# Optimization experiments

Measured on AMD Instinct MI355X. Metric: run time of the kernel, lower is better.

Reference implementation:

```python
import jax, jax.numpy as jnp
import numpy as np
from jax import lax

# MuSc core (post-ViT): multiscale avg-pooled patch features -> mutual pairwise
# distance scoring (leave-one-out over batch) -> top-min-k mean -> pixel map.
L_LAYERS = 4      # len(feature_layers)
B = 8             # batch (mutual-scoring reference pool)
PH = PW = 24      # 336 / patch 14
P = PH * PW       # 576 patches
D = 1024          # ViT-L embed dim
H = W = 336       # input image size
R_LIST = (1, 3, 5)
TOPMIN_MIN = 0.0
TOPMIN_MAX = 0.3


def setup_inputs() -> dict:
    key = jax.random.key(0)
    features = jax.random.normal(key, (L_LAYERS, B, P, D), dtype=jnp.float32)
    return {"features": features}


def _avg_pool_r(x, r):
    # x: [L, B, P, D]; AvgPool2d(r, stride=1, pad=r//2, count_include_pad=True)
    if r == 1:
        return x
    Ln, Bn, Pn, Dn = x.shape
    g = x.reshape(Ln, Bn, PH, PW, Dn)
    pad = r // 2
    s = lax.reduce_window(g, 0.0, lax.add,
                          (1, 1, r, r, 1), (1, 1, 1, 1, 1),
                          ((0, 0), (0, 0), (pad, pad), (pad, pad), (0, 0)))
    return (s / (r * r)).reshape(Ln, Bn, Pn, Dn)


def _msm_scores(feat):
    # feat: [L, B, P, D] L2-normalized. Mutual scoring (leave-one-out over B).
    sq = jnp.sum(feat * feat, axis=-1)                       # [L,B,P]
    dots = jnp.einsum('lbpd,lcqd->lbpcq', feat, feat)        # [L,B,P,B,P]
    d2 = sq[:, :, :, None, None] + sq[:, None, None, :, :] - 2.0 * dots
    d = jnp.sqrt(jnp.maximum(d2, 0.0))
    dmin = jnp.min(d, axis=-1)                               # [L,B,P,C] min over ref patches
    self_mask = jnp.eye(B, dtype=bool)[:, None, :]           # [B,1,C] exclude self image
    dmin = jnp.where(self_mask[None], jnp.inf, dmin)
    ds = jnp.sort(dmin, axis=-1)                             # ascending; self (inf) last
    ref = B - 1
    k_min = int(TOPMIN_MIN * ref)
    k_max = max(int(TOPMIN_MAX * ref), k_min + 1)
    return jnp.mean(ds[..., k_min:k_max], axis=-1)           # [L,B,P]


def _bilinear_ac(x, out_h, out_w):
    # align_corners=True bilinear upsample, x: [B, ph, pw]
    Bn, ph, pw = x.shape
    ys = jnp.arange(out_h, dtype=jnp.float32) * ((ph - 1) / (out_h - 1))
    xs = jnp.arange(out_w, dtype=jnp.float32) * ((pw - 1) / (out_w - 1))
    y0 = jnp.floor(ys).astype(jnp.int32); y1 = jnp.minimum(y0 + 1, ph - 1)
    x0 = jnp.floor(xs).astype(jnp.int32); x1 = jnp.minimum(x0 + 1, pw - 1)
    wy = (ys - y0)[None, :, None]
    wx = (xs - x0)[None, None, :]
    f00 = x[:, y0[:, None], x0[None, :]]
    f01 = x[:, y0[:, None], x1[None, :]]
    f10 = x[:, y1[:, None], x0[None, :]]
    f11 = x[:, y1[:, None], x1[None, :]]
    return (f00 * (1 - wy) * (1 - wx) + f01 * (1 - wy) * wx
            + f10 * wy * (1 - wx) + f11 * wy * wx)


def _forward(features):
    scores_r = []
    for r in R_LIST:  # small fixed multiscale loop
        f = _avg_pool_r(features, r)
        f = f / jnp.linalg.norm(f, axis=-1, keepdims=True)
        s = _msm_scores(f)                    # [L,B,P]
        scores_r.append(jnp.mean(s, axis=0))  # [B,P] mean over layers
    scores = jnp.mean(jnp.stack(scores_r, 0), axis=0)  # [B,P] mean over r
    scores_image = jnp.max(scores, axis=1)              # [B]
    scores_pixel = _bilinear_ac(scores.reshape(-1, PH, PW), H, W)  # [B,H,W]
    return scores_image, scores_pixel


def reference(features):
    return _forward(features)
```

## Files before the change

kernel.cpp:

```cpp
#include <hip/hip_runtime.h>
#include <stdint.h>

#define L_LAYERS 4
#define BATCH 8
#define PHH 24
#define PWW 24
#define PP (PHH*PWW)
#define DD 1024
#define ROWS (BATCH*PP)
#define OH 336
#define OW 336
#define NTILES 72
#define TT 36
#define NPAIRS (TT*(TT+1)/2)
#define NCOMBO 12
#define TOTBLK (NPAIRS*NCOMBO)
#define PRESCALE 1024.0f
#define INV_PRESCALE2_X2 (1.f/524288.f)

typedef __attribute__((ext_vector_type(8))) int i32x8;
typedef __attribute__((ext_vector_type(4))) float f32x4;

__device__ __forceinline__ unsigned int f2bf(float f) {
  unsigned int u = __float_as_uint(f);
  return (u + 0x7FFFu + ((u >> 16) & 1u)) >> 16;
}

__device__ __forceinline__ void load4bf(float* d, const unsigned short* p) {
  const uint2 u = *(const uint2*)p;
  d[0] = __uint_as_float(u.x << 16);
  d[1] = __uint_as_float(u.x & 0xFFFF0000u);
  d[2] = __uint_as_float(u.y << 16);
  d[3] = __uint_as_float(u.y & 0xFFFF0000u);
}

__device__ __forceinline__ void async16(const void* g, void* l) {
  __builtin_amdgcn_global_load_lds(
      (const __attribute__((address_space(1))) void*)(size_t)(uintptr_t)g,
      (__attribute__((address_space(3))) void*)(uint32_t)(uintptr_t)l,
      16, 0, 0);
}

__global__ __launch_bounds__(256) void vpool_ring_kernel(
    const float* __restrict__ feat,
    unsigned short* __restrict__ c3,
    unsigned short* __restrict__ c5) {
  const int dch = blockIdx.x;
  const int b = blockIdx.y;
  const int l = blockIdx.z >> 1;
  const int half = blockIdx.z & 1;
  const int py0 = half * 12, py1 = py0 + 11;
  const int t = threadIdx.x;
  const int pxg = t >> 5;
  const int d2 = t & 31;

  __shared__ float ring[5][24 * 64];

  const float* fb = feat + ((size_t)l * BATCH + b) * PP * DD + dch * 64 + d2 * 2;

  for (int yy = py0 - 2; yy <= py0 + 1; ++yy) {
    if (yy < 0) continue;
    #pragma unroll
    for (int i = 0; i < 3; ++i) {
      int px = i * 8 + pxg;
      *(float2*)&ring[yy % 5][px * 64 + d2 * 2] =
          *(const float2*)(fb + (size_t)(yy * PWW + px) * DD);
    }
  }
  for (int py = py0; py <= py1; ++py) {
    const int yl = py + 2;
    if (yl < PHH) {
      __syncthreads();
      #pragma unroll
      for (int i = 0; i < 3; ++i) {
        int px = i * 8 + pxg;
        *(float2*)&ring[yl % 5][px * 64 + d2 * 2] =
            *(const float2*)(fb + (size_t)(yl * PWW + px) * DD);
      }
    }
    __syncthreads();
    #pragma unroll
    for (int i = 0; i < 3; ++i) {
      int px = i * 8 + pxg;
      float s3x = 0.f, s3y = 0.f, s5x = 0.f, s5y = 0.f;
      #pragma unroll
      for (int dy = -2; dy <= 2; ++dy) {
        int yy = py + dy;
        if (yy < 0 || yy >= PHH) continue;
        float2 v = *(const float2*)&ring[yy % 5][px * 64 + d2 * 2];
        s5x += v.x; s5y += v.y;
        if (dy >= -1 && dy <= 1) { s3x += v.x; s3y += v.y; }
      }
      const size_t idx =
          ((size_t)l * ROWS + b * PP + py * PWW + px) * DD + dch * 64 + d2 * 2;
      *(unsigned int*)&c3[idx] = f2bf(s3x) | (f2bf(s3y) << 16);
      *(unsigned int*)&c5[idx] = f2bf(s5x) | (f2bf(s5y) << 16);
    }
  }
}

__global__ __launch_bounds__(256) void hpool_slide_kernel(
    const float* __restrict__ feat,
    const unsigned short* __restrict__ c3,
    const unsigned short* __restrict__ c5,
    unsigned char* __restrict__ nf_all) {
  const int rb = blockIdx.x;
  const int l = blockIdx.y;
  const int b = rb / PHH, py = rb % PHH;
  const int t = threadIdx.x;
  const int lane = t & 63, w = t >> 6;
  const int d0 = t * 4;
  const size_t rowbase = (size_t)b * PP + (size_t)py * PWW;

  const float* fb = feat + ((size_t)l * BATCH * PP + rowbase) * DD + d0;
  const unsigned short* c3b = c3 + ((size_t)l * ROWS + rowbase) * DD + d0;
  const unsigned short* c5b = c5 + ((size_t)l * ROWS + rowbase) * DD + d0;
  unsigned char* nf1 = nf_all + (((size_t)(0*L_LAYERS + l) * ROWS + rowbase) * DD + d0);
  unsigned char* nf3 = nf_all + (((size_t)(1*L_LAYERS + l) * ROWS + rowbase) * DD + d0);
  unsigned char* nf5 = nf_all + (((size_t)(2*L_LAYERS + l) * ROWS + rowbase) * DD + d0);

  float w3[3][4] = {{0,0,0,0},{0,0,0,0},{0,0,0,0}};
  float w5[5][4] = {{0,0,0,0},{0,0,0,0},{0,0,0,0},{0,0,0,0},{0,0,0,0}};
  load4bf(w3[1], c3b);
  load4bf(w3[2], c3b + DD);
  load4bf(w5[2], c5b);
  load4bf(w5[3], c5b + DD);
  load4bf(w5[4], c5b + 2 * DD);

  __shared__ float red[4][3];

  for (int px = 0; px < PWW; ++px) {
    float s1[4], s3[4], s5[4];
    const float4 f = *(const float4*)(fb + (size_t)px * DD);
    s1[0] = f.x; s1[1] = f.y; s1[2] = f.z; s1[3] = f.w;
    #pragma unroll
    for (int j = 0; j < 4; ++j) {
      s3[j] = w3[0][j] + w3[1][j] + w3[2][j];
      s5[j] = w5[0][j] + w5[1][j] + w5[2][j] + w5[3][j] + w5[4][j];
    }
    float q1 = 0, q3 = 0, q5 = 0;
    #pragma unroll
    for (int j = 0; j < 4; ++j) {
      q1 += s1[j]*s1[j]; q3 += s3[j]*s3[j]; q5 += s5[j]*s5[j];
    }
    #pragma unroll
    for (int off = 32; off > 0; off >>= 1) {
      q1 += __shfl_down(q1, off);
      q3 += __shfl_down(q3, off);
      q5 += __shfl_down(q5, off);
    }
    __syncthreads();
    if (lane == 0) { red[w][0] = q1; red[w][1] = q3; red[w][2] = q5; }
    __syncthreads();
    const float rn1 = rsqrtf(red[0][0] + red[1][0] + red[2][0] + red[3][0]) * PRESCALE;
    const float rn3 = rsqrtf(red[0][1] + red[1][1] + red[2][1] + red[3][1]) * PRESCALE;
    const float rn5 = rsqrtf(red[0][2] + red[1][2] + red[2][2] + red[3][2]) * PRESCALE;

    const size_t po = (size_t)px * DD;
    unsigned int o;
    o = __builtin_amdgcn_cvt_pk_fp8_f32(s1[0]*rn1, s1[1]*rn1, 0, false);
    o = __builtin_amdgcn_cvt_pk_fp8_f32(s1[2]*rn1, s1[3]*rn1, o, true);
    *(unsigned int*)(nf1 + po) = o;
    o = __builtin_amdgcn_cvt_pk_fp8_f32(s3[0]*rn3, s3[1]*rn3, 0, false);
    o = __builtin_amdgcn_cvt_pk_fp8_f32(s3[2]*rn3, s3[3]*rn3, o, true);
    *(unsigned int*)(nf3 + po) = o;
    o = __builtin_amdgcn_cvt_pk_fp8_f32(s5[0]*rn5, s5[1]*rn5, 0, false);
    o = __builtin_amdgcn_cvt_pk_fp8_f32(s5[2]*rn5, s5[3]*rn5, o, true);
    *(unsigned int*)(nf5 + po) = o;

    #pragma unroll
    for (int j = 0; j < 4; ++j) { w3[0][j] = w3[1][j]; w3[1][j] = w3[2][j]; }
    if (px + 2 < PWW) load4bf(w3[2], c3b + (size_t)(px + 2) * DD);
    else { w3[2][0]=0; w3[2][1]=0; w3[2][2]=0; w3[2][3]=0; }
    #pragma unroll
    for (int i = 0; i < 4; ++i)
      #pragma unroll
      for (int j = 0; j < 4; ++j) w5[i][j] = w5[i+1][j];
    if (px + 3 < PWW) load4bf(w5[4], c5b + (size_t)(px + 3) * DD);
    else { w5[4][0]=0; w5[4][1]=0; w5[4][2]=0; w5[4][3]=0; }
  }
}

__global__ __launch_bounds__(256, 3) void gemm_max_kernel(
    const unsigned char* __restrict__ nf_all,
    float* __restrict__ part) {
  const int bid = blockIdx.x;
  const int slot = (bid & 7) * (TOTBLK / 8) + (bid >> 3);
  const int combo = slot / NPAIRS;
  int rem = slot % NPAIRS;
  int it = 0;
  while (rem >= TT - it) { rem -= TT - it; ++it; }
  const int jt = it + rem;
  const int row0 = it * 128;
  const int col0 = jt * 128;

  {
    const bool inA = (row0 / PP) == ((row0 + 127) / PP);
    const bool inB = (col0 / PP) == ((col0 + 127) / PP);
    if (inA && inB && (row0 / PP) == (col0 / PP)) return;
  }

  __shared__ unsigned char As[128 * 128];
  __shared__ unsigned char Bs[128 * 128];

  const int t = threadIdx.x;
  const int lane = t & 63;
  const int wave = t >> 6;
  const int wm = wave >> 1;
  const int wn = wave & 1;

  const unsigned char* nf = nf_all + (size_t)combo * ROWS * DD;
  float* partialL = part + (size_t)combo * ROWS * NTILES;

  const f32x4 zero = {0.f, 0.f, 0.f, 0.f};
  f32x4 acc[4][4];
  #pragma unroll
  for (int m = 0; m < 4; ++m)
    #pragma unroll
    for (int n = 0; n < 4; ++n) acc[m][n] = zero;

  const unsigned char* gA = nf + (size_t)row0 * DD;
  const unsigned char* gB = nf + (size_t)col0 * DD;

  const int r15 = lane & 15;
  const int loff = ((((lane >> 4) << 1) ^ (r15 & 6)) << 4);
  const unsigned char* Abase = As + (size_t)(wm * 64 + r15) * 128 + loff;
  const unsigned char* Bbase = Bs + (size_t)(wn * 64 + r15) * 128 + loff;

  for (int kt = 0; kt < DD / 128; ++kt) {
    const int k0 = kt * 128;
    #pragma unroll
    for (int i = 0; i < 4; ++i) {
      int c = i * 256 + t;
      int row = c >> 3, j = c & 7;
      int g = j ^ (row & 6);
      async16(gA + (size_t)row * DD + k0 + g * 16, &As[c * 16]);
    }
    #pragma unroll
    for (int i = 0; i < 4; ++i) {
      int c = i * 256 + t;
      int row = c >> 3, j = c & 7;
      int g = j ^ (row & 6);
      async16(gB + (size_t)row * DD + k0 + g * 16, &Bs[c * 16]);
    }
    __syncthreads();

    const i32x8 a0 = *(const i32x8*)(Abase +    0);
    const i32x8 a1 = *(const i32x8*)(Abase + 2048);
    const i32x8 a2 = *(const i32x8*)(Abase + 4096);
    const i32x8 a3 = *(const i32x8*)(Abase + 6144);
    #pragma unroll
    for (int n = 0; n < 4; ++n) {
      const i32x8 bn = *(const i32x8*)(Bbase + n * 2048);
      acc[0][n] = __builtin_amdgcn_mfma_scale_f32_16x16x128_f8f6f4(
          a0, bn, acc[0][n], 0, 0, 0, 0x7F7F7F7F, 0, 0x7F7F7F7F);
      acc[1][n] = __builtin_amdgcn_mfma_scale_f32_16x16x128_f8f6f4(
          a1, bn, acc[1][n], 0, 0, 0, 0x7F7F7F7F, 0, 0x7F7F7F7F);
      acc[2][n] = __builtin_amdgcn_mfma_scale_f32_16x16x128_f8f6f4(
          a2, bn, acc[2][n], 0, 0, 0, 0x7F7F7F7F, 0, 0x7F7F7F7F);
      acc[3][n] = __builtin_amdgcn_mfma_scale_f32_16x16x128_f8f6f4(
          a3, bn, acc[3][n], 0, 0, 0, 0x7F7F7F7F, 0, 0x7F7F7F7F);
    }
    __syncthreads();
  }

  #pragma unroll
  for (int m = 0; m < 4; ++m) {
    #pragma unroll
    for (int g = 0; g < 4; ++g) {
      float v = fmaxf(fmaxf(acc[m][0][g], acc[m][1][g]),
                      fmaxf(acc[m][2][g], acc[m][3][g]));
      v = fmaxf(v, __shfl_xor(v, 1));
      v = fmaxf(v, __shfl_xor(v, 2));
      v = fmaxf(v, __shfl_xor(v, 4));
      v = fmaxf(v, __shfl_xor(v, 8));
      if ((lane & 15) == 0) {
        int row = row0 + wm * 64 + m * 16 + (lane >> 4) * 4 + g;
        partialL[(size_t)row * NTILES + 2 * jt + wn] = v;
      }
    }
  }
  if (it != jt) {
    #pragma unroll
    for (int n = 0; n < 4; ++n) {
      float v = -1e30f;
      #pragma unroll
      for (int m = 0; m < 4; ++m)
        #pragma unroll
        for (int g = 0; g < 4; ++g) v = fmaxf(v, acc[m][n][g]);
      v = fmaxf(v, __shfl_xor(v, 16));
      v = fmaxf(v, __shfl_xor(v, 32));
      if (lane < 16) {
        int col = col0 + wn * 64 + n * 16 + lane;
        partialL[(size_t)col * NTILES + 2 * it + wm] = v;
      }
    }
  }
}

__global__ __launch_bounds__(256) void reduce_topk_kernel(
    const float* __restrict__ part,
    float* __restrict__ scores) {
  const int row = blockIdx.x * 256 + threadIdx.x;
  if (row >= ROWS) return;
  const int b = row / PP;
  float sum = 0.f;
  for (int k = 0; k < NCOMBO; ++k) {
    const float* pr = part + ((size_t)k * ROWS + row) * NTILES;
    float d1 = 1e30f, d2 = 1e30f;
    #pragma unroll
    for (int c = 0; c < BATCH; ++c) {
      if (c == b) continue;
      float md = pr[c * 9];
      #pragma unroll
      for (int q = 1; q < 9; ++q) md = fmaxf(md, pr[c * 9 + q]);
      float d = sqrtf(fmaxf(2.f - md * INV_PRESCALE2_X2, 0.f));
      if (d < d1) { d2 = d1; d1 = d; }
      else if (d < d2) { d2 = d; }
    }
    sum += 0.5f * (d1 + d2);
  }
  scores[row] = sum;
}

__global__ __launch_bounds__(256) void image_max_kernel(
    const float* __restrict__ scores, float* __restrict__ out) {
  const int b = blockIdx.x;
  const int t = threadIdx.x;
  float m = -1e30f;
  for (int p = t; p < PP; p += 256) m = fmaxf(m, scores[b * PP + p]);
  #pragma unroll
  for (int off = 32; off > 0; off >>= 1) m = fmaxf(m, __shfl_down(m, off));
  __shared__ float red[4];
  if ((t & 63) == 0) red[t >> 6] = m;
  __syncthreads();
  if (t == 0)
    out[b] = fmaxf(fmaxf(red[0], red[1]), fmaxf(red[2], red[3])) * (1.f / 12.f);
}

__global__ __launch_bounds__(256) void upsample_kernel(
    const float* __restrict__ scores, float* __restrict__ out) {
  const int idx = blockIdx.x * 256 + threadIdx.x;
  if (idx >= BATCH * OH * OW) return;
  const int b = idx / (OH * OW);
  const int rem = idx % (OH * OW);
  const int y = rem / OW, x = rem % OW;
  const float sc = (float)(23.0 / 335.0);
  const float ys = y * sc, xs = x * sc;
  const int y0 = (int)floorf(ys), x0 = (int)floorf(xs);
  const float wy = ys - (float)y0, wx = xs - (float)x0;
  const int y1 = min(y0 + 1, PHH - 1), x1 = min(x0 + 1, PWW - 1);
  const float* sb = scores + b * PP;
  const float f00 = sb[y0 * PWW + x0], f01 = sb[y0 * PWW + x1];
  const float f10 = sb[y1 * PWW + x0], f11 = sb[y1 * PWW + x1];
  const float v = f00 * (1.f - wy) * (1.f - wx) + f01 * (1.f - wy) * wx +
                  f10 * wy * (1.f - wx) + f11 * wy * wx;
  out[8 + idx] = v * (1.f / 12.f);
}

extern "C" void kernel_launch(void* const* d_in, const int* in_sizes, int n_in,
                              void* d_out, int out_size, void* d_ws, size_t ws_size,
                              hipStream_t stream) {
  const float* feat = (const float*)d_in[0];
  float* out = (float*)d_out;
  char* ws = (char*)d_ws;

  const size_t NF_BYTES   = (size_t)NCOMBO * ROWS * DD;
  const size_t PART_BYTES = (size_t)NCOMBO * ROWS * NTILES * 4;
  const size_t SCR_BYTES  = (size_t)ROWS * 4;
  const size_t C_BYTES    = (size_t)L_LAYERS * ROWS * DD * 2;
  unsigned char*  nf_all = (unsigned char*)ws;
  float*          part   = (float*)(ws + NF_BYTES);
  float*          scr    = (float*)(ws + NF_BYTES + PART_BYTES);
  unsigned short* c3     = (unsigned short*)(ws + NF_BYTES + PART_BYTES + SCR_BYTES);
  unsigned short* c5     = (unsigned short*)(ws + NF_BYTES + PART_BYTES + SCR_BYTES + C_BYTES);

  vpool_ring_kernel<<<dim3(16, BATCH, L_LAYERS * 2), 256, 0, stream>>>(feat, c3, c5);
  hpool_slide_kernel<<<dim3(PHH * BATCH, L_LAYERS), 256, 0, stream>>>(feat, c3, c5, nf_all);
  gemm_max_kernel<<<TOTBLK, 256, 0, stream>>>(nf_all, part);
  reduce_topk_kernel<<<(ROWS + 255) / 256, 256, 0, stream>>>(part, scr);
  image_max_kernel<<<BATCH, 256, 0, stream>>>(scr, out);
  upsample_kernel<<<(BATCH * OH * OW + 255) / 256, 256, 0, stream>>>(scr, out);
}
```

Baseline: 368.6 us.

## Move horizontal pooling into vertical pool kernel and parallelize quantization per row

The vertical pooling kernel now also does the horizontal 3/5 box sum through a shared-memory row buffer, so the pooled 2D sums are written once. The second pass becomes a per-row normalize-and-quantize kernel launched with one block per row and layer, replacing the serial sliding-window loop that synchronized 24 times per block. The image-max and upsample kernels are merged into one launch. The vertical sums are rounded to bf16 before the horizontal sum, which adds an extra rounding step, and the pool kernel gains an extra barrier per row.

```diff
diff --git a/kernel.cpp b/kernel.cpp
--- a/kernel.cpp
+++ b/kernel.cpp
@@ -26,12 +26,17 @@
   return (u + 0x7FFFu + ((u >> 16) & 1u)) >> 16;
 }
 
+__device__ __forceinline__ float bflo(unsigned int w) {
+  return __uint_as_float(w << 16);
+}
+__device__ __forceinline__ float bfhi(unsigned int w) {
+  return __uint_as_float(w & 0xFFFF0000u);
+}
+
 __device__ __forceinline__ void load4bf(float* d, const unsigned short* p) {
   const uint2 u = *(const uint2*)p;
-  d[0] = __uint_as_float(u.x << 16);
-  d[1] = __uint_as_float(u.x & 0xFFFF0000u);
-  d[2] = __uint_as_float(u.y << 16);
-  d[3] = __uint_as_float(u.y & 0xFFFF0000u);
+  d[0] = bflo(u.x); d[1] = bfhi(u.x);
+  d[2] = bflo(u.y); d[3] = bfhi(u.y);
 }
 
 __device__ __forceinline__ void async16(const void* g, void* l) {
@@ -41,10 +46,10 @@
       16, 0, 0);
 }
 
-__global__ __launch_bounds__(256) void vpool_ring_kernel(
+__global__ __launch_bounds__(256) void pool_kernel(
     const float* __restrict__ feat,
-    unsigned short* __restrict__ c3,
-    unsigned short* __restrict__ c5) {
+    unsigned short* __restrict__ h3,
+    unsigned short* __restrict__ h5) {
   const int dch = blockIdx.x;
   const int b = blockIdx.y;
   const int l = blockIdx.z >> 1;
@@ -55,6 +60,8 @@
   const int d2 = t & 31;
 
   __shared__ float ring[5][24 * 64];
+  __shared__ unsigned int v3p[24 * 32];
+  __shared__ unsigned int v5p[24 * 32];
 
   const float* fb = feat + ((size_t)l * BATCH + b) * PP * DD + dch * 64 + d2 * 2;
 
@@ -91,94 +98,82 @@
         s5x += v.x; s5y += v.y;
         if (dy >= -1 && dy <= 1) { s3x += v.x; s3y += v.y; }
       }
+      v3p[px * 32 + d2] = f2bf(s3x) | (f2bf(s3y) << 16);
+      v5p[px * 32 + d2] = f2bf(s5x) | (f2bf(s5y) << 16);
+    }
+    __syncthreads();
+    #pragma unroll
+    for (int i = 0; i < 3; ++i) {
+      int px = i * 8 + pxg;
+      float h3x = 0.f, h3y = 0.f, h5x = 0.f, h5y = 0.f;
+      #pragma unroll
+      for (int dx = -2; dx <= 2; ++dx) {
+        int xx = px + dx;
+        if (xx < 0 || xx >= PWW) continue;
+        unsigned int w5 = v5p[xx * 32 + d2];
+        h5x += bflo(w5); h5y += bfhi(w5);
+        if (dx >= -1 && dx <= 1) {
+          unsigned int w3 = v3p[xx * 32 + d2];
+          h3x += bflo(w3); h3y += bfhi(w3);
+        }
+      }
       const size_t idx =
           ((size_t)l * ROWS + b * PP + py * PWW + px) * DD + dch * 64 + d2 * 2;
-      *(unsigned int*)&c3[idx] = f2bf(s3x) | (f2bf(s3y) << 16);
-      *(unsigned int*)&c5[idx] = f2bf(s5x) | (f2bf(s5y) << 16);
-    }
-  }
-}
-
-__global__ __launch_bounds__(256) void hpool_slide_kernel(
+      *(unsigned int*)&h3[idx] = f2bf(h3x) | (f2bf(h3y) << 16);
+      *(unsigned int*)&h5[idx] = f2bf(h5x) | (f2bf(h5y) << 16);
+    }
+  }
+}
+
+__global__ __launch_bounds__(256) void quant_kernel(
     const float* __restrict__ feat,
-    const unsigned short* __restrict__ c3,
-    const unsigned short* __restrict__ c5,
+    const unsigned short* __restrict__ h3,
+    const unsigned short* __restrict__ h5,
     unsigned char* __restrict__ nf_all) {
-  const int rb = blockIdx.x;
+  const int row = blockIdx.x;
   const int l = blockIdx.y;
-  const int b = rb / PHH, py = rb % PHH;
   const int t = threadIdx.x;
   const int lane = t & 63, w = t >> 6;
   const int d0 = t * 4;
-  const size_t rowbase = (size_t)b * PP + (size_t)py * PWW;
-
-  const float* fb = feat + ((size_t)l * BATCH * PP + rowbase) * DD + d0;
-  const unsigned short* c3b = c3 + ((size_t)l * ROWS + rowbase) * DD + d0;
-  const unsigned short* c5b = c5 + ((size_t)l * ROWS + rowbase) * DD + d0;
-  unsigned char* nf1 = nf_all + (((size_t)(0*L_LAYERS + l) * ROWS + rowbase) * DD + d0);
-  unsigned char* nf3 = nf_all + (((size_t)(1*L_LAYERS + l) * ROWS + rowbase) * DD + d0);
-  unsigned char* nf5 = nf_all + (((size_t)(2*L_LAYERS + l) * ROWS + rowbase) * DD + d0);
-
-  float w3[3][4] = {{0,0,0,0},{0,0,0,0},{0,0,0,0}};
-  float w5[5][4] = {{0,0,0,0},{0,0,0,0},{0,0,0,0},{0,0,0,0},{0,0,0,0}};
-  load4bf(w3[1], c3b);
-  load4bf(w3[2], c3b + DD);
-  load4bf(w5[2], c5b);
-  load4bf(w5[3], c5b + DD);
-  load4bf(w5[4], c5b + 2 * DD);
-
+  const size_t lro = ((size_t)l * ROWS + row) * DD + d0;
+
+  float s1[4], s3[4], s5[4];
+  {
+    const float4 f = *(const float4*)(feat + lro);
+    s1[0] = f.x; s1[1] = f.y; s1[2] = f.z; s1[3] = f.w;
+  }
+  load4bf(s3, h3 + lro);
+  load4bf(s5, h5 + lro);
+
+  float q1 = 0.f, q3 = 0.f, q5 = 0.f;
+  #pragma unroll
+  for (int j = 0; j < 4; ++j) {
+    q1 += s1[j]*s1[j]; q3 += s3[j]*s3[j]; q5 += s5[j]*s5[j];
+  }
+  #pragma unroll
+  for (int off = 32; off > 0; off >>= 1) {
+    q1 += __shfl_down(q1, off);
+    q3 += __shfl_down(q3, off);
+    q5 += __shfl_down(q5, off);
+  }
   __shared__ float red[4][3];
-
-  for (int px = 0; px < PWW; ++px) {
-    float s1[4], s3[4], s5[4];
-    const float4 f = *(const float4*)(fb + (size_t)px * DD);
-    s1[0] = f.x; s1[1] = f.y; s1[2] = f.z; s1[3] = f.w;
-    #pragma unroll
-    for (int j = 0; j < 4; ++j) {
-      s3[j] = w3[0][j] + w3[1][j] + w3[2][j];
-      s5[j] = w5[0][j] + w5[1][j] + w5[2][j] + w5[3][j] + w5[4][j];
-    }
-    float q1 = 0, q3 = 0, q5 = 0;
-    #pragma unroll
-    for (int j = 0; j < 4; ++j) {
-      q1 += s1[j]*s1[j]; q3 += s3[j]*s3[j]; q5 += s5[j]*s5[j];
-    }
-    #pragma unroll
-    for (int off = 32; off > 0; off >>= 1) {
-      q1 += __shfl_down(q1, off);
-      q3 += __shfl_down(q3, off);
-      q5 += __shfl_down(q5, off);
-    }
-    __syncthreads();
-    if (lane == 0) { red[w][0] = q1; red[w][1] = q3; red[w][2] = q5; }
-    __syncthreads();
-    const float rn1 = rsqrtf(red[0][0] + red[1][0] + red[2][0] + red[3][0]) * PRESCALE;
-    const float rn3 = rsqrtf(red[0][1] + red[1][1] + red[2][1] + red[3][1]) * PRESCALE;
-    const float rn5 = rsqrtf(red[0][2] + red[1][2] + red[2][2] + red[3][2]) * PRESCALE;
-
-    const size_t po = (size_t)px * DD;
-    unsigned int o;
-    o = __builtin_amdgcn_cvt_pk_fp8_f32(s1[0]*rn1, s1[1]*rn1, 0, false);
-    o = __builtin_amdgcn_cvt_pk_fp8_f32(s1[2]*rn1, s1[3]*rn1, o, true);
-    *(unsigned int*)(nf1 + po) = o;
-    o = __builtin_amdgcn_cvt_pk_fp8_f32(s3[0]*rn3, s3[1]*rn3, 0, false);
-    o = __builtin_amdgcn_cvt_pk_fp8_f32(s3[2]*rn3, s3[3]*rn3, o, true);
-    *(unsigned int*)(nf3 + po) = o;
-    o = __builtin_amdgcn_cvt_pk_fp8_f32(s5[0]*rn5, s5[1]*rn5, 0, false);
-    o = __builtin_amdgcn_cvt_pk_fp8_f32(s5[2]*rn5, s5[3]*rn5, o, true);
-    *(unsigned int*)(nf5 + po) = o;
-
-    #pragma unroll
-    for (int j = 0; j < 4; ++j) { w3[0][j] = w3[1][j]; w3[1][j] = w3[2][j]; }
-    if (px + 2 < PWW) load4bf(w3[2], c3b + (size_t)(px + 2) * DD);
-    else { w3[2][0]=0; w3[2][1]=0; w3[2][2]=0; w3[2][3]=0; }
-    #pragma unroll
-    for (int i = 0; i < 4; ++i)
-      #pragma unroll
-      for (int j = 0; j < 4; ++j) w5[i][j] = w5[i+1][j];
-    if (px + 3 < PWW) load4bf(w5[4], c5b + (size_t)(px + 3) * DD);
-    else { w5[4][0]=0; w5[4][1]=0; w5[4][2]=0; w5[4][3]=0; }
-  }
+  if (lane == 0) { red[w][0] = q1; red[w][1] = q3; red[w][2] = q5; }
+  __syncthreads();
+  const float rn1 = rsqrtf(red[0][0] + red[1][0] + red[2][0] + red[3][0]) * PRESCALE;
+  const float rn3 = rsqrtf(red[0][1] + red[1][1] + red[2][1] + red[3][1]) * PRESCALE;
+  const float rn5 = rsqrtf(red[0][2] + red[1][2] + red[2][2] + red[3][2]) * PRESCALE;
+
+  const size_t ro = (size_t)row * DD + d0;
+  unsigned int o;
+  o = __builtin_amdgcn_cvt_pk_fp8_f32(s1[0]*rn1, s1[1]*rn1, 0, false);
+  o = __builtin_amdgcn_cvt_pk_fp8_f32(s1[2]*rn1, s1[3]*rn1, o, true);
+  *(unsigned int*)(nf_all + (size_t)(0*L_LAYERS + l) * ROWS * DD + ro) = o;
+  o = __builtin_amdgcn_cvt_pk_fp8_f32(s3[0]*rn3, s3[1]*rn3, 0, false);
+  o = __builtin_amdgcn_cvt_pk_fp8_f32(s3[2]*rn3, s3[3]*rn3, o, true);
+  *(unsigned int*)(nf_all + (size_t)(1*L_LAYERS + l) * ROWS * DD + ro) = o;
+  o = __builtin_amdgcn_cvt_pk_fp8_f32(s5[0]*rn5, s5[1]*rn5, 0, false);
+  o = __builtin_amdgcn_cvt_pk_fp8_f32(s5[2]*rn5, s5[3]*rn5, o, true);
+  *(unsigned int*)(nf_all + (size_t)(2*L_LAYERS + l) * ROWS * DD + ro) = o;
 }
 
 __global__ __launch_bounds__(256, 3) void gemm_max_kernel(
@@ -323,39 +318,38 @@
   scores[row] = sum;
 }
 
-__global__ __launch_bounds__(256) void image_max_kernel(
+__global__ __launch_bounds__(256) void final_kernel(
     const float* __restrict__ scores, float* __restrict__ out) {
-  const int b = blockIdx.x;
+  const int bid = blockIdx.x;
   const int t = threadIdx.x;
-  float m = -1e30f;
-  for (int p = t; p < PP; p += 256) m = fmaxf(m, scores[b * PP + p]);
-  #pragma unroll
-  for (int off = 32; off > 0; off >>= 1) m = fmaxf(m, __shfl_down(m, off));
-  __shared__ float red[4];
-  if ((t & 63) == 0) red[t >> 6] = m;
-  __syncthreads();
-  if (t == 0)
-    out[b] = fmaxf(fmaxf(red[0], red[1]), fmaxf(red[2], red[3])) * (1.f / 12.f);
-}
-
-__global__ __launch_bounds__(256) void upsample_kernel(
-    const float* __restrict__ scores, float* __restrict__ out) {
-  const int idx = blockIdx.x * 256 + threadIdx.x;
-  if (idx >= BATCH * OH * OW) return;
-  const int b = idx / (OH * OW);
-  const int rem = idx % (OH * OW);
-  const int y = rem / OW, x = rem % OW;
-  const float sc = (float)(23.0 / 335.0);
-  const float ys = y * sc, xs = x * sc;
-  const int y0 = (int)floorf(ys), x0 = (int)floorf(xs);
-  const float wy = ys - (float)y0, wx = xs - (float)x0;
-  const int y1 = min(y0 + 1, PHH - 1), x1 = min(x0 + 1, PWW - 1);
-  const float* sb = scores + b * PP;
-  const float f00 = sb[y0 * PWW + x0], f01 = sb[y0 * PWW + x1];
-  const float f10 = sb[y1 * PWW + x0], f11 = sb[y1 * PWW + x1];
-  const float v = f00 * (1.f - wy) * (1.f - wx) + f01 * (1.f - wy) * wx +
-                  f10 * wy * (1.f - wx) + f11 * wy * wx;
-  out[8 + idx] = v * (1.f / 12.f);
+  if (bid < (BATCH * OH * OW) / 256) {
+    const int idx = bid * 256 + t;
+    const int b = idx / (OH * OW);
+    const int rem = idx % (OH * OW);
+    const int y = rem / OW, x = rem % OW;
+    const float sc = (float)(23.0 / 335.0);
+    const float ys = y * sc, xs = x * sc;
+    const int y0 = (int)floorf(ys), x0 = (int)floorf(xs);
+    const float wy = ys - (float)y0, wx = xs - (float)x0;
+    const int y1 = min(y0 + 1, PHH - 1), x1 = min(x0 + 1, PWW - 1);
+    const float* sb = scores + b * PP;
+    const float f00 = sb[y0 * PWW + x0], f01 = sb[y0 * PWW + x1];
+    const float f10 = sb[y1 * PWW + x0], f11 = sb[y1 * PWW + x1];
+    const float v = f00 * (1.f - wy) * (1.f - wx) + f01 * (1.f - wy) * wx +
+                    f10 * wy * (1.f - wx) + f11 * wy * wx;
+    out[8 + idx] = v * (1.f / 12.f);
+  } else {
+    const int b = bid - (BATCH * OH * OW) / 256;
+    float m = -1e30f;
+    for (int p = t; p < PP; p += 256) m = fmaxf(m, scores[b * PP + p]);
+    #pragma unroll
+    for (int off = 32; off > 0; off >>= 1) m = fmaxf(m, __shfl_down(m, off));
+    __shared__ float red[4];
+    if ((t & 63) == 0) red[t >> 6] = m;
+    __syncthreads();
+    if (t == 0)
+      out[b] = fmaxf(fmaxf(red[0], red[1]), fmaxf(red[2], red[3])) * (1.f / 12.f);
+  }
 }
 
 extern "C" void kernel_launch(void* const* d_in, const int* in_sizes, int n_in,
@@ -368,17 +362,16 @@
   const size_t NF_BYTES   = (size_t)NCOMBO * ROWS * DD;
   const size_t PART_BYTES = (size_t)NCOMBO * ROWS * NTILES * 4;
   const size_t SCR_BYTES  = (size_t)ROWS * 4;
-  const size_t C_BYTES    = (size_t)L_LAYERS * ROWS * DD * 2;
+  const size_t H_BYTES    = (size_t)L_LAYERS * ROWS * DD * 2;
   unsigned char*  nf_all = (unsigned char*)ws;
   float*          part   = (float*)(ws + NF_BYTES);
   float*          scr    = (float*)(ws + NF_BYTES + PART_BYTES);
-  unsigned short* c3     = (unsigned short*)(ws + NF_BYTES + PART_BYTES + SCR_BYTES);
-  unsigned short* c5     = (unsigned short*)(ws + NF_BYTES + PART_BYTES + SCR_BYTES + C_BYTES);
-
-  vpool_ring_kernel<<<dim3(16, BATCH, L_LAYERS * 2), 256, 0, stream>>>(feat, c3, c5);
-  hpool_slide_kernel<<<dim3(PHH * BATCH, L_LAYERS), 256, 0, stream>>>(feat, c3, c5, nf_all);
+  unsigned short* h3     = (unsigned short*)(ws + NF_BYTES + PART_BYTES + SCR_BYTES);
+  unsigned short* h5     = (unsigned short*)(ws + NF_BYTES + PART_BYTES + SCR_BYTES + H_BYTES);
+
+  pool_kernel<<<dim3(16, BATCH, L_LAYERS * 2), 256, 0, stream>>>(feat, h3, h5);
+  quant_kernel<<<dim3(ROWS, L_LAYERS), 256, 0, stream>>>(feat, h3, h5, nf_all);
   gemm_max_kernel<<<TOTBLK, 256, 0, stream>>>(nf_all, part);
   reduce_topk_kernel<<<(ROWS + 255) / 256, 256, 0, stream>>>(part, scr);
-  image_max_kernel<<<BATCH, 256, 0, stream>>>(scr, out);
-  upsample_kernel<<<(BATCH * OH * OW + 255) / 256, 256, 0, stream>>>(scr, out);
-}
+  final_kernel<<<(BATCH * OH * OW) / 256 + BATCH, 256, 0, stream>>>(scr, out);
+}
```

Result: faster. 360.9 us (-2.1%).
